# Optimization experiments

Hardware: AMD Instinct MI355X
Metric: run time of the kernel (lower is better)

Reference implementation:

```python
import jax, jax.numpy as jnp
import numpy as np

N_NODES = 50000


def setup_inputs() -> dict:
    key = jax.random.key(0)
    k1, k2, k3, k4 = jax.random.split(key, 4)
    in_f, out_f = 128, 128
    n_edges = 625000
    x = jax.random.normal(k1, (N_NODES, in_f), dtype=jnp.float32)
    index = jax.random.randint(k2, (2, n_edges), 0, N_NODES, dtype=jnp.int64)
    # reset_parameters uses uniform(-1/sqrt(in), 1/sqrt(in))
    bound = 1.0 / np.sqrt(in_f)
    weight = jax.random.uniform(k3, (in_f, out_f), minval=-bound, maxval=bound, dtype=jnp.float32)
    bias = jax.random.uniform(k4, (out_f,), minval=-bound, maxval=bound, dtype=jnp.float32)
    return {"x": x, "index": index, "weight": weight, "bias": bias}


def reference(x, index, weight, bias):
    # F_out = D_hat^{-1/2} (A + I) D_hat^{-1/2} X W + b
    n = x.shape[0]
    loops = jnp.arange(n, dtype=index.dtype)
    src = jnp.concatenate([index[0], loops])  # [E + N]
    dst = jnp.concatenate([index[1], loops])
    # degrees of A_hat (counted on destination nodes)
    deg = jax.ops.segment_sum(jnp.ones_like(dst, dtype=x.dtype), dst, num_segments=n)
    dinv = jax.lax.rsqrt(jnp.maximum(deg, 1e-12))
    norm = dinv[src] * dinv[dst]  # [E + N]
    h = x @ weight  # [N, out] dense GEMM first (out <= in)
    msg = h[src] * norm[:, None]  # gather + scale
    out = jax.ops.segment_sum(msg, dst, num_segments=n)  # scatter-add
    return out + bias
```

## Files before the change

kernel.cpp:

```cpp
#include <hip/hip_runtime.h>

#define F   128
#define PAD 64

typedef short short8 __attribute__((ext_vector_type(8)));
typedef float f32x4v __attribute__((ext_vector_type(4)));

__device__ __forceinline__ ushort f2bf(float f) {
    uint b = __float_as_uint(f);
    uint r = (b + 0x7fffu + ((b >> 16) & 1u)) >> 16;
    return (ushort)r;
}
__device__ __forceinline__ float bflo(uint v) { return __uint_as_float(v << 16); }
__device__ __forceinline__ float bfhi(uint v) { return __uint_as_float(v & 0xffff0000u); }


__global__ __launch_bounds__(256) void hybrid(
    const int* __restrict__ src, const int* __restrict__ dst, int ne,
    int* __restrict__ cnt, ushort* __restrict__ padded, int nbB,
    const float* __restrict__ x, const float* __restrict__ w,
    ushort* __restrict__ g, int n)
{
    if (blockIdx.x < nbB) {
        int e = blockIdx.x * 256 + threadIdx.x;
        if (e < ne) {
            int s = src[e], d = dst[e];
            int p = atomicAdd(&cnt[d], 1);
            if (p < PAD) padded[(size_t)d * PAD + p] = (ushort)s;
        }
        return;
    }

    const int gb   = blockIdx.x - nbB;
    const int t    = threadIdx.x;
    const int lane = t & 63;
    const int wv   = t >> 6;
    const int wr   = wv >> 1, wc = wv & 1;
    const int l15  = lane & 15, kg = lane >> 4;
    const int row0 = gb * 64 + wr * 32;
    const int col0 = wc * 64;

    f32x4v acc[2][4];
    #pragma unroll
    for (int rt = 0; rt < 2; ++rt)
        #pragma unroll
        for (int ct = 0; ct < 4; ++ct)
            acc[rt][ct] = (f32x4v){0.f, 0.f, 0.f, 0.f};

    #pragma unroll
    for (int kt = 0; kt < 4; ++kt) {
        const int k0 = kt * 32 + kg * 8;
        short8 a[2];
        #pragma unroll
        for (int rt = 0; rt < 2; ++rt) {
            int row = row0 + rt * 16 + l15;
            row = row < n ? row : n - 1;
            float4 p0 = *reinterpret_cast<const float4*>(&x[(size_t)row * F + k0]);
            float4 p1 = *reinterpret_cast<const float4*>(&x[(size_t)row * F + k0 + 4]);
            ushort u[8] = {f2bf(p0.x), f2bf(p0.y), f2bf(p0.z), f2bf(p0.w),
                           f2bf(p1.x), f2bf(p1.y), f2bf(p1.z), f2bf(p1.w)};
            a[rt] = *reinterpret_cast<short8*>(u);
        }
        short8 b[4];
        #pragma unroll
        for (int ct = 0; ct < 4; ++ct) {
            int col = col0 + ct * 16 + l15;
            ushort u[8];
            #pragma unroll
            for (int j = 0; j < 8; ++j)
                u[j] = f2bf(w[(size_t)(k0 + j) * F + col]);
            b[ct] = *reinterpret_cast<short8*>(u);
        }
        #pragma unroll
        for (int rt = 0; rt < 2; ++rt)
            #pragma unroll
            for (int ct = 0; ct < 4; ++ct)
                acc[rt][ct] = __builtin_amdgcn_mfma_f32_16x16x32_bf16(
                    a[rt], b[ct], acc[rt][ct], 0, 0, 0);
    }

    #pragma unroll
    for (int rt = 0; rt < 2; ++rt) {
        int rbase = row0 + rt * 16 + kg * 4;
        #pragma unroll
        for (int ct = 0; ct < 4; ++ct) {
            int col = col0 + ct * 16 + l15;
            #pragma unroll
            for (int rr = 0; rr < 4; ++rr) {
                int row = rbase + rr;
                if (row < n)
                    g[(size_t)row * F + col] = f2bf(acc[rt][ct][rr]);
            }
        }
    }
}


__global__ __launch_bounds__(256) void gather_bf16(
    const int* __restrict__ cnt, const ushort* __restrict__ padded,
    const ushort* __restrict__ g, const float* __restrict__ bias,
    float* __restrict__ out, int n)
{
    int wid  = (blockIdx.x * 256 + threadIdx.x) >> 6;
    int lane = threadIdx.x & 63;
    if (wid >= n) return;
    wid = __builtin_amdgcn_readfirstlane(wid);
    const int c = lane * 2;

    int   cv = cnt[wid];
    float dv = rsqrtf((float)cv + 1.0f);
    uint self = *reinterpret_cast<const uint*>(&g[(size_t)wid * F + c]);
    float ax = dv * bflo(self), ay = dv * bfhi(self);

    int m = cv < PAD ? cv : PAD;
    const ushort* pl = padded + (size_t)wid * PAD;

    int j = 0;
    for (; j + 4 <= m; j += 4) {
        int s0 = pl[j + 0], s1 = pl[j + 1], s2 = pl[j + 2], s3 = pl[j + 3];
        float d0 = rsqrtf((float)cnt[s0] + 1.0f);
        float d1 = rsqrtf((float)cnt[s1] + 1.0f);
        float d2 = rsqrtf((float)cnt[s2] + 1.0f);
        float d3 = rsqrtf((float)cnt[s3] + 1.0f);
        uint v0 = *reinterpret_cast<const uint*>(&g[(size_t)s0 * F + c]);
        uint v1 = *reinterpret_cast<const uint*>(&g[(size_t)s1 * F + c]);
        uint v2 = *reinterpret_cast<const uint*>(&g[(size_t)s2 * F + c]);
        uint v3 = *reinterpret_cast<const uint*>(&g[(size_t)s3 * F + c]);
        ax = fmaf(d0, bflo(v0), ax); ay = fmaf(d0, bfhi(v0), ay);
        ax = fmaf(d1, bflo(v1), ax); ay = fmaf(d1, bfhi(v1), ay);
        ax = fmaf(d2, bflo(v2), ax); ay = fmaf(d2, bfhi(v2), ay);
        ax = fmaf(d3, bflo(v3), ax); ay = fmaf(d3, bfhi(v3), ay);
    }
    for (; j < m; ++j) {
        int s = pl[j];
        float ds = rsqrtf((float)cnt[s] + 1.0f);
        uint v = *reinterpret_cast<const uint*>(&g[(size_t)s * F + c]);
        ax = fmaf(ds, bflo(v), ax);
        ay = fmaf(ds, bfhi(v), ay);
    }

    float2 bb = *reinterpret_cast<const float2*>(&bias[c]);
    float2 o;
    o.x = fmaf(dv, ax, bb.x);
    o.y = fmaf(dv, ay, bb.y);
    *reinterpret_cast<float2*>(&out[(size_t)wid * F + c]) = o;
}


__global__ __launch_bounds__(256) void gemm_scale(
    const float* __restrict__ x, const float* __restrict__ w,
    const float* __restrict__ dinv, float* __restrict__ g, int n)
{
    __shared__ float sWl[F * F];
    __shared__ float sXl[8][F];
    for (int i = threadIdx.x; i < F * F; i += 256) sWl[i] = w[i];
    __syncthreads();
    const int r  = threadIdx.x >> 5;
    const int cg = threadIdx.x & 31;
    for (int row0 = blockIdx.x * 8; row0 < n; row0 += gridDim.x * 8) {
        {
            int t4 = threadIdx.x * 4;
            int rr = t4 >> 7, cc = t4 & (F - 1);
            if (row0 + rr < n) {
                float4 v = *reinterpret_cast<const float4*>(&x[(size_t)(row0 + rr) * F + cc]);
                *reinterpret_cast<float4*>(&sXl[rr][cc]) = v;
            }
        }
        __syncthreads();
        int row = row0 + r;
        if (row < n) {
            float4 acc = make_float4(0.f, 0.f, 0.f, 0.f);
            const float* xr = sXl[r];
            #pragma unroll 8
            for (int k = 0; k < F; ++k) {
                float  xv = xr[k];
                float4 wv = *reinterpret_cast<const float4*>(&sWl[k * F + cg * 4]);
                acc.x = fmaf(xv, wv.x, acc.x);
                acc.y = fmaf(xv, wv.y, acc.y);
                acc.z = fmaf(xv, wv.z, acc.z);
                acc.w = fmaf(xv, wv.w, acc.w);
            }
            float s = dinv[row];
            acc.x *= s; acc.y *= s; acc.z *= s; acc.w *= s;
            *reinterpret_cast<float4*>(&g[(size_t)row * F + cg * 4]) = acc;
        }
        __syncthreads();
    }
}

__global__ void init_degf(float* __restrict__ deg, int n) {
    int i = blockIdx.x * blockDim.x + threadIdx.x;
    if (i < n) deg[i] = 1.0f;
}
__global__ void count_degf(const int* __restrict__ dst, int ne, float* __restrict__ deg) {
    int e = blockIdx.x * blockDim.x + threadIdx.x;
    if (e < ne) atomicAdd(&deg[dst[e]], 1.0f);
}
__global__ void calc_dinvf(const float* __restrict__ deg, float* __restrict__ dinv, int n) {
    int i = blockIdx.x * blockDim.x + threadIdx.x;
    if (i < n) dinv[i] = rsqrtf(fmaxf(deg[i], 1e-12f));
}
__global__ __launch_bounds__(256) void scatter_edges(
    const int* __restrict__ src, const int* __restrict__ dst, int ne,
    const float* __restrict__ g, float* __restrict__ out)
{
    int gid  = (blockIdx.x * blockDim.x + threadIdx.x) >> 5;
    int lane = threadIdx.x & 31;
    if (gid >= ne) return;
    int s = src[gid], d = dst[gid];
    float4 v = *reinterpret_cast<const float4*>(&g[(size_t)s * F + lane * 4]);
    float* op = &out[(size_t)d * F + lane * 4];
    atomicAdd(op + 0, v.x);
    atomicAdd(op + 1, v.y);
    atomicAdd(op + 2, v.z);
    atomicAdd(op + 3, v.w);
}
__global__ __launch_bounds__(256) void finalize(
    float* __restrict__ out, const float* __restrict__ g,
    const float* __restrict__ dinv, const float* __restrict__ bias, int n)
{
    int i = blockIdx.x * blockDim.x + threadIdx.x;
    if (i >= n * 32) return;
    int row = i >> 5, c4 = i & 31;
    float  s = dinv[row];
    float4 o = *reinterpret_cast<float4*>(&out[(size_t)i * 4]);
    float4 gg = *reinterpret_cast<const float4*>(&g[(size_t)i * 4]);
    float4 b = *reinterpret_cast<const float4*>(&bias[c4 * 4]);
    o.x = fmaf(s, o.x + gg.x, b.x);
    o.y = fmaf(s, o.y + gg.y, b.y);
    o.z = fmaf(s, o.z + gg.z, b.z);
    o.w = fmaf(s, o.w + gg.w, b.w);
    *reinterpret_cast<float4*>(&out[(size_t)i * 4]) = o;
}


extern "C" void kernel_launch(void* const* d_in, const int* in_sizes, int n_in,
                              void* d_out, int out_size, void* d_ws, size_t ws_size,
                              hipStream_t stream) {
    const float* x     = (const float*)d_in[0];
    const int*   index = (const int*)d_in[1];
    const float* w     = (const float*)d_in[2];
    const float* bias  = (const float*)d_in[3];
    float*       out   = (float*)d_out;

    int n  = in_sizes[0] / F;
    int ne = in_sizes[1] / 2;
    const int* src = index;
    const int* dst = index + ne;

    size_t b_cnt    = 0;
    size_t b_padded = (b_cnt + (size_t)n * 4 + 15) & ~(size_t)15;
    size_t b_g      = (b_padded + (size_t)n * PAD * 2 + 15) & ~(size_t)15;
    size_t need     = b_g + (size_t)n * F * 2;

    char* wsb = (char*)d_ws;
    int*    cnt    = (int*)(wsb + b_cnt);
    ushort* padded = (ushort*)(wsb + b_padded);
    ushort* g      = (ushort*)(wsb + b_g);

    int nbB = (ne + 255) / 256;
    int nbG = (n + 63) / 64;

    if (ws_size >= need && n <= 65535) {
        hipMemsetAsync(cnt, 0, (size_t)n * 4, stream);
        hybrid<<<nbB + nbG, 256, 0, stream>>>(src, dst, ne, cnt, padded, nbB, x, w, g, n);
        int gb = (int)(((long long)n * 64 + 255) / 256);
        gather_bf16<<<gb, 256, 0, stream>>>(cnt, padded, g, bias, out, n);
    } else {
        float* degf  = (float*)wsb;
        float* dinvf = (float*)wsb + n;
        float* gf    = (float*)wsb + 2 * n;
        int nb  = (n + 255) / 256;
        int nbE = (ne + 255) / 256;
        hipMemsetAsync(d_out, 0, (size_t)out_size * sizeof(float), stream);
        init_degf<<<nb, 256, 0, stream>>>(degf, n);
        count_degf<<<nbE, 256, 0, stream>>>(dst, ne, degf);
        calc_dinvf<<<nb, 256, 0, stream>>>(degf, dinvf, n);
        gemm_scale<<<(n + 7) / 8, 256, 0, stream>>>(x, w, dinvf, gf, n);
        int sc_blocks = (int)(((long long)ne * 32 + 255) / 256);
        scatter_edges<<<sc_blocks, 256, 0, stream>>>(src, dst, ne, gf, out);
        finalize<<<(n * 32 + 255) / 256, 256, 0, stream>>>(out, gf, dinvf, bias, n);
    }
}
```

Before: 100.0 us.

## Replace padded per-node adjacency with binned CSR built via scan and block-local sort

The fused degree-count/GEMM kernel now only counts degrees, vectorised four destinations at a time. A scan over 512-node bins and a binning scatter then pack (dst,src) pairs into per-bin segments. The gather kernel rebuilds per-node source lists in LDS for 128 nodes and accumulates bf16 rows. This removes the PAD=64 cap, so no edges are dropped, and replaces random per-node atomics with block-local ones. The cost is two extra launches, each bin segment being read twice by four blocks, and a single-block scan.

```diff
diff --git a/kernel.cpp b/kernel.cpp
--- a/kernel.cpp
+++ b/kernel.cpp
@@ -1,7 +1,9 @@
 #include <hip/hip_runtime.h>
 
-#define F   128
-#define PAD 64
+#define F     128
+#define BINW  512
+#define NBMAX 128
+#define LCAP  6144
 
 typedef short short8 __attribute__((ext_vector_type(8)));
 typedef float f32x4v __attribute__((ext_vector_type(4)));
@@ -16,22 +18,26 @@
 
 
 __global__ __launch_bounds__(256) void hybrid(
-    const int* __restrict__ src, const int* __restrict__ dst, int ne,
-    int* __restrict__ cnt, ushort* __restrict__ padded, int nbB,
+    const int* __restrict__ dst, int ne,
+    int* __restrict__ cnt, int nbH,
     const float* __restrict__ x, const float* __restrict__ w,
     ushort* __restrict__ g, int n)
 {
-    if (blockIdx.x < nbB) {
-        int e = blockIdx.x * 256 + threadIdx.x;
-        if (e < ne) {
-            int s = src[e], d = dst[e];
-            int p = atomicAdd(&cnt[d], 1);
-            if (p < PAD) padded[(size_t)d * PAD + p] = (ushort)s;
+    if (blockIdx.x < nbH) {
+        int base = (blockIdx.x * 256 + threadIdx.x) * 4;
+        if (base + 3 < ne) {
+            int4 d4 = *reinterpret_cast<const int4*>(&dst[base]);
+            atomicAdd(&cnt[d4.x], 1);
+            atomicAdd(&cnt[d4.y], 1);
+            atomicAdd(&cnt[d4.z], 1);
+            atomicAdd(&cnt[d4.w], 1);
+        } else {
+            for (int e = base; e < ne; ++e) atomicAdd(&cnt[dst[e]], 1);
         }
         return;
     }
 
-    const int gb   = blockIdx.x - nbB;
+    const int gb   = blockIdx.x - nbH;
     const int t    = threadIdx.x;
     const int lane = t & 63;
     const int wv   = t >> 6;
@@ -96,54 +102,180 @@
 }
 
 
-__global__ __launch_bounds__(256) void gather_bf16(
-    const int* __restrict__ cnt, const ushort* __restrict__ padded,
+__global__ __launch_bounds__(256) void scan_bins(
+    const int* __restrict__ cnt, int* __restrict__ binOff, int* __restrict__ bincur,
+    int n, int nbins)
+{
+    __shared__ int sB[NBMAX];
+    const int t = threadIdx.x;
+    int mysum = 0;
+    if (t < nbins) {
+        int lo = t * BINW;
+        int hi = lo + BINW < n ? lo + BINW : n;
+        int i = lo;
+        for (; i + 4 <= hi; i += 4) {
+            int4 c = *reinterpret_cast<const int4*>(&cnt[i]);
+            mysum += c.x + c.y + c.z + c.w;
+        }
+        for (; i < hi; ++i) mysum += cnt[i];
+    }
+    if (t < NBMAX) sB[t] = (t < nbins) ? mysum : 0;
+    __syncthreads();
+    for (int d = 1; d < NBMAX; d <<= 1) {
+        int v = 0;
+        if (t < NBMAX && t >= d) v = sB[t - d];
+        __syncthreads();
+        if (t < NBMAX) sB[t] += v;
+        __syncthreads();
+    }
+    if (t < nbins) {
+        int excl = sB[t] - mysum;
+        binOff[t] = excl;
+        bincur[t] = excl;
+    }
+}
+
+
+__global__ __launch_bounds__(256) void binscat(
+    const int* __restrict__ src, const int* __restrict__ dst, int ne,
+    int* __restrict__ bincur, uint* __restrict__ bindat, int nbins)
+{
+    __shared__ int bC[NBMAX];
+    __shared__ int bB[NBMAX];
+    const int t = threadIdx.x;
+    if (t < NBMAX) bC[t] = 0;
+    __syncthreads();
+
+    int e[8], s[8], d[8];
+    const int base = blockIdx.x * 2048;
+    #pragma unroll
+    for (int k = 0; k < 8; ++k) {
+        e[k] = base + t + k * 256;
+        if (e[k] < ne) {
+            s[k] = src[e[k]];
+            d[k] = dst[e[k]];
+            atomicAdd(&bC[d[k] >> 9], 1);
+        }
+    }
+    __syncthreads();
+    if (t < nbins && bC[t] > 0) {
+        bB[t] = atomicAdd(&bincur[t], bC[t]);
+    }
+    if (t < NBMAX) bC[t] = 0;
+    __syncthreads();
+    #pragma unroll
+    for (int k = 0; k < 8; ++k) {
+        if (e[k] < ne) {
+            int b = d[k] >> 9;
+            int pos = bB[b] + atomicAdd(&bC[b], 1);
+            bindat[pos] = ((uint)d[k] << 16) | (uint)s[k];
+        }
+    }
+}
+
+
+__global__ __launch_bounds__(256) void gather_bins(
+    const int* __restrict__ binOff, const int* __restrict__ bincur,
+    const uint* __restrict__ bindat, const int* __restrict__ cnt,
     const ushort* __restrict__ g, const float* __restrict__ bias,
     float* __restrict__ out, int n)
 {
-    int wid  = (blockIdx.x * 256 + threadIdx.x) >> 6;
-    int lane = threadIdx.x & 63;
-    if (wid >= n) return;
-    wid = __builtin_amdgcn_readfirstlane(wid);
-    const int c = lane * 2;
-
-    int   cv = cnt[wid];
-    float dv = rsqrtf((float)cv + 1.0f);
-    uint self = *reinterpret_cast<const uint*>(&g[(size_t)wid * F + c]);
-    float ax = dv * bflo(self), ay = dv * bfhi(self);
-
-    int m = cv < PAD ? cv : PAD;
-    const ushort* pl = padded + (size_t)wid * PAD;
-
-    int j = 0;
-    for (; j + 4 <= m; j += 4) {
-        int s0 = pl[j + 0], s1 = pl[j + 1], s2 = pl[j + 2], s3 = pl[j + 3];
-        float d0 = rsqrtf((float)cnt[s0] + 1.0f);
-        float d1 = rsqrtf((float)cnt[s1] + 1.0f);
-        float d2 = rsqrtf((float)cnt[s2] + 1.0f);
-        float d3 = rsqrtf((float)cnt[s3] + 1.0f);
-        uint v0 = *reinterpret_cast<const uint*>(&g[(size_t)s0 * F + c]);
-        uint v1 = *reinterpret_cast<const uint*>(&g[(size_t)s1 * F + c]);
-        uint v2 = *reinterpret_cast<const uint*>(&g[(size_t)s2 * F + c]);
-        uint v3 = *reinterpret_cast<const uint*>(&g[(size_t)s3 * F + c]);
-        ax = fmaf(d0, bflo(v0), ax); ay = fmaf(d0, bfhi(v0), ay);
-        ax = fmaf(d1, bflo(v1), ax); ay = fmaf(d1, bfhi(v1), ay);
-        ax = fmaf(d2, bflo(v2), ax); ay = fmaf(d2, bfhi(v2), ay);
-        ax = fmaf(d3, bflo(v3), ax); ay = fmaf(d3, bfhi(v3), ay);
-    }
-    for (; j < m; ++j) {
-        int s = pl[j];
-        float ds = rsqrtf((float)cnt[s] + 1.0f);
-        uint v = *reinterpret_cast<const uint*>(&g[(size_t)s * F + c]);
-        ax = fmaf(ds, bflo(v), ax);
-        ay = fmaf(ds, bfhi(v), ay);
-    }
-
-    float2 bb = *reinterpret_cast<const float2*>(&bias[c]);
-    float2 o;
-    o.x = fmaf(dv, ax, bb.x);
-    o.y = fmaf(dv, ay, bb.y);
-    *reinterpret_cast<float2*>(&out[(size_t)wid * F + c]) = o;
+    __shared__ ushort lsrc[LCAP];
+    __shared__ int cntL[128];
+    __shared__ int offL[128];
+    __shared__ int curL[128];
+
+    const int t     = threadIdx.x;
+    const int node0 = blockIdx.x * 128;
+    const int bin   = node0 >> 9;
+    const int segLo = binOff[bin];
+    const int segHi = bincur[bin];
+
+    if (t < 128) cntL[t] = 0;
+    __syncthreads();
+
+    for (int i = segLo + t; i < segHi; i += 256) {
+        uint e = bindat[i];
+        uint l = (e >> 16) - (uint)node0;
+        if (l < 128u) atomicAdd(&cntL[l], 1);
+    }
+    __syncthreads();
+
+    int myc = (t < 128) ? cntL[t] : 0;
+    if (t < 128) offL[t] = myc;
+    __syncthreads();
+    for (int d = 1; d < 128; d <<= 1) {
+        int v = 0;
+        if (t < 128 && t >= d) v = offL[t - d];
+        __syncthreads();
+        if (t < 128) offL[t] += v;
+        __syncthreads();
+    }
+    if (t < 128) {
+        int excl = offL[t] - myc;
+        offL[t] = excl;
+        curL[t] = excl;
+    }
+    __syncthreads();
+
+    for (int i = segLo + t; i < segHi; i += 256) {
+        uint e = bindat[i];
+        uint l = (e >> 16) - (uint)node0;
+        if (l < 128u) {
+            int p = atomicAdd(&curL[l], 1);
+            if (p < LCAP) lsrc[p] = (ushort)(e & 0xffffu);
+        }
+    }
+    __syncthreads();
+
+    const int wv   = t >> 6;
+    const int lane = t & 63;
+    const int c    = lane * 2;
+
+    for (int i = 0; i < 32; ++i) {
+        int l = wv * 32 + i;
+        int node = node0 + l;
+        if (node >= n) break;
+        int m   = cntL[l];
+        int off = offL[l];
+        float dv = rsqrtf((float)m + 1.0f);
+
+        uint self = *reinterpret_cast<const uint*>(&g[(size_t)node * F + c]);
+        float ax = dv * bflo(self), ay = dv * bfhi(self);
+
+        int j = 0;
+        for (; j + 4 <= m; j += 4) {
+            int s0 = __builtin_amdgcn_readfirstlane((int)lsrc[off + j + 0]);
+            int s1 = __builtin_amdgcn_readfirstlane((int)lsrc[off + j + 1]);
+            int s2 = __builtin_amdgcn_readfirstlane((int)lsrc[off + j + 2]);
+            int s3 = __builtin_amdgcn_readfirstlane((int)lsrc[off + j + 3]);
+            float d0 = rsqrtf((float)cnt[s0] + 1.0f);
+            float d1 = rsqrtf((float)cnt[s1] + 1.0f);
+            float d2 = rsqrtf((float)cnt[s2] + 1.0f);
+            float d3 = rsqrtf((float)cnt[s3] + 1.0f);
+            uint v0 = *reinterpret_cast<const uint*>(&g[(size_t)s0 * F + c]);
+            uint v1 = *reinterpret_cast<const uint*>(&g[(size_t)s1 * F + c]);
+            uint v2 = *reinterpret_cast<const uint*>(&g[(size_t)s2 * F + c]);
+            uint v3 = *reinterpret_cast<const uint*>(&g[(size_t)s3 * F + c]);
+            ax = fmaf(d0, bflo(v0), ax); ay = fmaf(d0, bfhi(v0), ay);
+            ax = fmaf(d1, bflo(v1), ax); ay = fmaf(d1, bfhi(v1), ay);
+            ax = fmaf(d2, bflo(v2), ax); ay = fmaf(d2, bfhi(v2), ay);
+            ax = fmaf(d3, bflo(v3), ax); ay = fmaf(d3, bfhi(v3), ay);
+        }
+        for (; j < m; ++j) {
+            int s = __builtin_amdgcn_readfirstlane((int)lsrc[off + j]);
+            float ds = rsqrtf((float)cnt[s] + 1.0f);
+            uint v = *reinterpret_cast<const uint*>(&g[(size_t)s * F + c]);
+            ax = fmaf(ds, bflo(v), ax);
+            ay = fmaf(ds, bfhi(v), ay);
+        }
+
+        float2 bb = *reinterpret_cast<const float2*>(&bias[c]);
+        float2 o;
+        o.x = fmaf(dv, ax, bb.x);
+        o.y = fmaf(dv, ay, bb.y);
+        *reinterpret_cast<float2*>(&out[(size_t)node * F + c]) = o;
+    }
 }
 
 
@@ -247,25 +379,33 @@
     int ne = in_sizes[1] / 2;
     const int* src = index;
     const int* dst = index + ne;
+    int nbins = (n + BINW - 1) / BINW;
 
     size_t b_cnt    = 0;
-    size_t b_padded = (b_cnt + (size_t)n * 4 + 15) & ~(size_t)15;
-    size_t b_g      = (b_padded + (size_t)n * PAD * 2 + 15) & ~(size_t)15;
+    size_t b_boff   = (b_cnt + (size_t)n * 4 + 15) & ~(size_t)15;
+    size_t b_bcur   = (b_boff + NBMAX * 4 + 15) & ~(size_t)15;
+    size_t b_bindat = (b_bcur + NBMAX * 4 + 15) & ~(size_t)15;
+    size_t b_g      = (b_bindat + (size_t)ne * 4 + 15) & ~(size_t)15;
     size_t need     = b_g + (size_t)n * F * 2;
 
     char* wsb = (char*)d_ws;
     int*    cnt    = (int*)(wsb + b_cnt);
-    ushort* padded = (ushort*)(wsb + b_padded);
+    int*    binOff = (int*)(wsb + b_boff);
+    int*    bincur = (int*)(wsb + b_bcur);
+    uint*   bindat = (uint*)(wsb + b_bindat);
     ushort* g      = (ushort*)(wsb + b_g);
 
-    int nbB = (ne + 255) / 256;
+    int nbH = (ne + 1023) / 1024;
     int nbG = (n + 63) / 64;
-
-    if (ws_size >= need && n <= 65535) {
+    int nbS = (ne + 2047) / 2048;
+    int nbK = (n + 127) / 128;
+
+    if (ws_size >= need && n <= 65536) {
         hipMemsetAsync(cnt, 0, (size_t)n * 4, stream);
-        hybrid<<<nbB + nbG, 256, 0, stream>>>(src, dst, ne, cnt, padded, nbB, x, w, g, n);
-        int gb = (int)(((long long)n * 64 + 255) / 256);
-        gather_bf16<<<gb, 256, 0, stream>>>(cnt, padded, g, bias, out, n);
+        hybrid<<<nbH + nbG, 256, 0, stream>>>(dst, ne, cnt, nbH, x, w, g, n);
+        scan_bins<<<1, 256, 0, stream>>>(cnt, binOff, bincur, n, nbins);
+        binscat<<<nbS, 256, 0, stream>>>(src, dst, ne, bincur, bindat, nbins);
+        gather_bins<<<nbK, 256, 0, stream>>>(binOff, bincur, bindat, cnt, g, bias, out, n);
     } else {
         float* degf  = (float*)wsb;
         float* dinvf = (float*)wsb + n;
```

Measured after the change: 172.9 us. 72.9% more time.
